# Optimization experiments

Hardware: AMD Instinct MI355X
Metric: run time of the kernel (lower is better)

Reference implementation:

```python
import jax, jax.numpy as jnp
import numpy as np

B, G, MAXITER = 8, 1024, 16
H = 1.0 / (G - 1)          # grid spacing h = (right-left)/(GridSize-1) on unit square
GD = 0.0                   # Dirichlet boundary value used by hard_encode padding

_K_CROSS = np.array([[0.0, 0.5, 0.0], [0.5, 0.0, 0.5], [0.0, 0.5, 0.0]], np.float32).reshape(1, 1, 3, 3)
_K3 = np.array([[0.0, 0.5, 0.0], [0.5, 2.0, 0.5], [0.0, 0.5, 0.0]], np.float32).reshape(1, 1, 3, 3)


def _conv3x3(x, k):
    # valid 3x3 conv, NCHW / OIHW (matches torch F.conv2d with no padding)
    return jax.lax.conv_general_dilated(x, k, (1, 1), 'VALID',
                                        dimension_numbers=('NCHW', 'OIHW', 'NCHW'))


def setup_inputs() -> dict:
    key = jax.random.key(0)
    k1, k2, k3 = jax.random.split(key, 3)
    pre = jax.random.normal(k1, (B, 1, G - 2, G - 2), dtype=jnp.float32)
    f = jax.random.normal(k2, (B, 1, G, G), dtype=jnp.float32)
    # positive coefficient field so the Jacobi divisor y3 stays bounded away from 0
    kappa = jax.random.uniform(k3, (B, 1, G, G), dtype=jnp.float32, minval=0.5, maxval=1.5)
    return {"pre": pre, "f": f, "kappa": kappa}


def reference(pre, f, kappa):
    kc = jnp.asarray(_K_CROSS, dtype=pre.dtype)
    k3 = jnp.asarray(_K3, dtype=pre.dtype)
    # loop-invariant terms: force = f_interior * h^2, w_interior, y3 = conv(w, k3)
    force = f[..., 1:-1, 1:-1] * (H * H)          # [B,1,G-2,G-2]
    w_in = kappa[..., 1:-1, 1:-1]                 # [B,1,G-2,G-2]
    y3 = _conv3x3(kappa, k3)                      # [B,1,G-2,G-2]

    def step(u, _):
        up = jnp.pad(u, ((0, 0), (0, 0), (1, 1), (1, 1)), constant_values=GD)  # hard_encode
        y1 = _conv3x3(up, kc) * w_in
        y2 = _conv3x3(kappa * up, kc)
        return (force + y1 + y2) / y3, None

    u, _ = jax.lax.scan(step, pre, None, length=MAXITER)
    return u
```

## Files before the change

### kernel.cpp

```cpp
#include <hip/hip_runtime.h>


namespace {
constexpr int    G    = 1024, Ni = 1022;
constexpr int    TOUT = 96, HALO = 16;
constexpr size_t IMG_K = (size_t)G * G;
constexpr size_t IMG_P = (size_t)Ni * Ni;
constexpr float  H2 = (float)(1.0 / (1023.0 * 1023.0));
}

__device__ __forceinline__ float frcp(float x) { return __builtin_amdgcn_rcpf(x); }

__device__ __forceinline__ float lane_shr1(float x) {
    return __builtin_bit_cast(float,
        __builtin_amdgcn_update_dpp(0, __builtin_bit_cast(int, x), 0x138, 0xF, 0xF, true));
}
__device__ __forceinline__ float lane_shl1(float x) {
    return __builtin_bit_cast(float,
        __builtin_amdgcn_update_dpp(0, __builtin_bit_cast(int, x), 0x130, 0xF, 0xF, true));
}

__global__ __launch_bounds__(1024, 4)
void jac_fused16(const float* __restrict__ pre, float* __restrict__ out,
                 const float* __restrict__ kap, const float* __restrict__ fin)
{
    __shared__ float2 ex[2][2][1024];

    const int tid = threadIdx.x;
    const int w = tid >> 6, l = tid & 63;
    const int bx = blockIdx.x, by = blockIdx.y, b = blockIdx.z;
    const int X0 = bx * TOUT - HALO, Y0 = by * TOUT - HALO;
    const int c0 = X0 + 2 * l;
    const int gy0 = Y0 + 8 * w;

    const float* kB = kap + (size_t)b * IMG_K;
    const float* fB = fin + (size_t)b * IMG_K;
    const bool fast = (bx >= 1) && (bx <= 9) && (by >= 1) && (by <= 9);

    float2 wN[8], wS[8], wW[8], wE[8], Fc[8];
    if (fast) {
        const float* kp = kB + (size_t)gy0 * G + c0;
        const float* fp = fB + (size_t)(gy0 + 1) * G + c0;
        float2 q0 = *(const float2*)kp;
        float2 q1 = *(const float2*)(kp + G);
        float  e0 = lane_shl1(q0.x);
        float  e1 = lane_shl1(q1.x);
        #pragma unroll
        for (int r = 0; r < 8; ++r) {
            const float2 q2 = *(const float2*)(kp + (size_t)(r + 2) * G);
            const float  e2 = lane_shl1(q2.x);
            const float2 fr = *(const float2*)(fp + (size_t)r * G);
            const float f0 = fr.y, f1 = lane_shl1(fr.x);
            const float ke1 = lane_shl1(q1.y);
            const float inv0 = frcp(2.0f * q1.y + 0.5f * (q0.y + q2.y + q1.x + e1));
            const float inv1 = frcp(2.0f * e1   + 0.5f * (e0 + e2 + q1.y + ke1));
            wN[r] = make_float2(0.5f * (q1.y + q0.y) * inv0, 0.5f * (e1 + e0) * inv1);
            wS[r] = make_float2(0.5f * (q1.y + q2.y) * inv0, 0.5f * (e1 + e2) * inv1);
            wW[r] = make_float2(0.5f * (q1.y + q1.x) * inv0, 0.5f * (e1 + q1.y) * inv1);
            wE[r] = make_float2(0.5f * (q1.y + e1)   * inv0, 0.5f * (e1 + ke1) * inv1);
            Fc[r] = make_float2(f0 * H2 * inv0, f1 * H2 * inv1);
            q0 = q1; q1 = q2; e0 = e1; e1 = e2;
        }
    } else {
        auto gk = [&](int ry, int cx) -> float {
            return ((unsigned)ry < (unsigned)G && (unsigned)cx < (unsigned)G)
                 ? kB[(size_t)ry * G + cx] : 0.0f;
        };
        float qx0 = gk(gy0,     c0), qy0 = gk(gy0,     c0 + 1);
        float qx1 = gk(gy0 + 1, c0), qy1 = gk(gy0 + 1, c0 + 1);
        float e0 = lane_shl1(qx0), e1 = lane_shl1(qx1);
        #pragma unroll
        for (int r = 0; r < 8; ++r) {
            const float qx2 = gk(gy0 + r + 2, c0), qy2 = gk(gy0 + r + 2, c0 + 1);
            const float e2 = lane_shl1(qx2);
            const int ry = gy0 + 1 + r;
            const bool rv = (unsigned)ry < (unsigned)G;
            const float fa = (rv && (unsigned)c0       < (unsigned)G) ? fB[(size_t)ry * G + c0]     : 0.0f;
            const float fb = (rv && (unsigned)(c0 + 1) < (unsigned)G) ? fB[(size_t)ry * G + c0 + 1] : 0.0f;
            const float f0 = fb, f1 = lane_shl1(fa);
            const float ke1 = lane_shl1(qy1);
            const float inv0 = frcp(2.0f * qy1 + 0.5f * (qy0 + qy2 + qx1 + e1));
            const float inv1 = frcp(2.0f * e1  + 0.5f * (e0 + e2 + qy1 + ke1));
            const int gy = gy0 + r;
            const bool dr = (unsigned)gy < (unsigned)Ni;
            const bool d0 = dr && (unsigned)c0       < (unsigned)Ni;
            const bool d1 = dr && (unsigned)(c0 + 1) < (unsigned)Ni;
            wN[r] = make_float2(d0 ? 0.5f * (qy1 + qy0) * inv0 : 0.0f,
                                d1 ? 0.5f * (e1 + e0)   * inv1 : 0.0f);
            wS[r] = make_float2(d0 ? 0.5f * (qy1 + qy2) * inv0 : 0.0f,
                                d1 ? 0.5f * (e1 + e2)   * inv1 : 0.0f);
            wW[r] = make_float2(d0 ? 0.5f * (qy1 + qx1) * inv0 : 0.0f,
                                d1 ? 0.5f * (e1 + qy1)  * inv1 : 0.0f);
            wE[r] = make_float2(d0 ? 0.5f * (qy1 + e1)  * inv0 : 0.0f,
                                d1 ? 0.5f * (e1 + ke1)  * inv1 : 0.0f);
            Fc[r] = make_float2(d0 ? f0 * H2 * inv0 : 0.0f,
                                d1 ? f1 * H2 * inv1 : 0.0f);
            qx0 = qx1; qy0 = qy1; qx1 = qx2; qy1 = qy2; e0 = e1; e1 = e2;
        }
    }

    float2 u[8];
    if (fast) {
        const float* uS = pre + (size_t)b * IMG_P + (size_t)gy0 * Ni + c0;
        #pragma unroll
        for (int r = 0; r < 8; ++r) u[r] = *(const float2*)(uS + (size_t)r * Ni);
    } else {
        const float* uS = pre + (size_t)b * IMG_P;
        #pragma unroll
        for (int r = 0; r < 8; ++r) {
            const int gy = gy0 + r;
            const bool rv = (unsigned)gy < (unsigned)Ni;
            const float a = (rv && (unsigned)c0       < (unsigned)Ni) ? uS[(size_t)gy * Ni + c0]     : 0.0f;
            const float q = (rv && (unsigned)(c0 + 1) < (unsigned)Ni) ? uS[(size_t)gy * Ni + c0 + 1] : 0.0f;
            u[r] = make_float2(a, q);
        }
    }

    const int iN = (w > 0)  ? tid - 64 : tid;
    const int iS = (w < 15) ? tid + 64 : tid;
    #pragma unroll
    for (int t = 0; t < 16; ++t) {
        float2* top = ex[t & 1][0];
        float2* bot = ex[t & 1][1];
        top[tid] = u[0];
        bot[tid] = u[7];
        __syncthreads();
        const float2 hN = bot[iN];
        const float2 hS = top[iS];
        float2 pn = hN;
        #pragma unroll
        for (int r = 0; r < 8; ++r) {
            const float2 s = (r < 7) ? u[r + 1] : hS;
            const float o0 = u[r].x, o1 = u[r].y;
            const float uW = lane_shr1(o1);
            const float uE = lane_shl1(o0);
            const float v0 = fmaf(wN[r].x, pn.x,
                             fmaf(wS[r].x, s.x,
                             fmaf(wW[r].x, uW,
                             fmaf(wE[r].x, o1, Fc[r].x))));
            const float v1 = fmaf(wN[r].y, pn.y,
                             fmaf(wS[r].y, s.y,
                             fmaf(wW[r].y, o0,
                             fmaf(wE[r].y, uE, Fc[r].y))));
            pn = make_float2(o0, o1);
            u[r] = make_float2(v0, v1);
        }
    }

    if (w >= 2 && w < 14 && l >= 8 && l < 56) {
        float* oB = out + (size_t)b * IMG_P;
        if (fast) {
            #pragma unroll
            for (int r = 0; r < 8; ++r)
                *(float2*)(oB + (size_t)(gy0 + r) * Ni + c0) = u[r];
        } else {
            #pragma unroll
            for (int r = 0; r < 8; ++r) {
                const int gy = gy0 + r;
                if ((unsigned)gy < (unsigned)Ni) {
                    if ((unsigned)c0       < (unsigned)Ni) oB[(size_t)gy * Ni + c0]     = u[r].x;
                    if ((unsigned)(c0 + 1) < (unsigned)Ni) oB[(size_t)gy * Ni + c0 + 1] = u[r].y;
                }
            }
        }
    }
}

extern "C" void kernel_launch(void* const* d_in, const int* in_sizes, int n_in,
                              void* d_out, int out_size, void* d_ws, size_t ws_size,
                              hipStream_t stream)
{
    const float* pre = (const float*)d_in[0];
    const float* f   = (const float*)d_in[1];
    const float* kap = (const float*)d_in[2];
    float* out = (float*)d_out;
    (void)d_ws; (void)ws_size;

    dim3 blk(1024, 1, 1);
    dim3 grd((Ni + TOUT - 1) / TOUT, (Ni + TOUT - 1) / TOUT, 8);

    jac_fused16<<<grd, blk, 0, stream>>>(pre, out, kap, f);
}
```

Baseline: 197.5 us.

## Eliminate east stencil weight via unit-sum identity and relax launch bounds

The four Jacobi neighbour weights sum to one, so the east weight is dropped. Each update is rewritten as the east neighbour plus weighted differences to the other neighbours, which frees the per-row wE registers. Boundary tiles lose the zero-weight trick for the east term, so a per-element mask array and a separate masked instantiation of the time loop are added. The launch bounds change from a min-blocks hint to an explicit waves-per-EU of 4, changing the register budget the compiler targets. The cost is extra subtractions per point, slightly different rounding from the rcp-based weights, and the mask multiplies on boundary tiles.

```diff
diff --git a/kernel.cpp b/kernel.cpp
--- a/kernel.cpp
+++ b/kernel.cpp
@@ -20,7 +20,8 @@
         __builtin_amdgcn_update_dpp(0, __builtin_bit_cast(int, x), 0x130, 0xF, 0xF, true));
 }
 
-__global__ __launch_bounds__(1024, 4)
+__global__ __launch_bounds__(1024)
+__attribute__((amdgpu_waves_per_eu(4, 4)))
 void jac_fused16(const float* __restrict__ pre, float* __restrict__ out,
                  const float* __restrict__ kap, const float* __restrict__ fin)
 {
@@ -37,7 +38,8 @@
     const float* fB = fin + (size_t)b * IMG_K;
     const bool fast = (bx >= 1) && (bx <= 9) && (by >= 1) && (by <= 9);
 
-    float2 wN[8], wS[8], wW[8], wE[8], Fc[8];
+    float2 wN[8], wS[8], wW[8], Fc[8];
+    float2 mk[8];
     if (fast) {
         const float* kp = kB + (size_t)gy0 * G + c0;
         const float* fp = fB + (size_t)(gy0 + 1) * G + c0;
@@ -57,7 +59,6 @@
             wN[r] = make_float2(0.5f * (q1.y + q0.y) * inv0, 0.5f * (e1 + e0) * inv1);
             wS[r] = make_float2(0.5f * (q1.y + q2.y) * inv0, 0.5f * (e1 + e2) * inv1);
             wW[r] = make_float2(0.5f * (q1.y + q1.x) * inv0, 0.5f * (e1 + q1.y) * inv1);
-            wE[r] = make_float2(0.5f * (q1.y + e1)   * inv0, 0.5f * (e1 + ke1) * inv1);
             Fc[r] = make_float2(f0 * H2 * inv0, f1 * H2 * inv1);
             q0 = q1; q1 = q2; e0 = e1; e1 = e2;
         }
@@ -66,6 +67,8 @@
             return ((unsigned)ry < (unsigned)G && (unsigned)cx < (unsigned)G)
                  ? kB[(size_t)ry * G + cx] : 0.0f;
         };
+        const float cm0 = ((unsigned)c0       < (unsigned)Ni) ? 1.0f : 0.0f;
+        const float cm1 = ((unsigned)(c0 + 1) < (unsigned)Ni) ? 1.0f : 0.0f;
         float qx0 = gk(gy0,     c0), qy0 = gk(gy0,     c0 + 1);
         float qx1 = gk(gy0 + 1, c0), qy1 = gk(gy0 + 1, c0 + 1);
         float e0 = lane_shl1(qx0), e1 = lane_shl1(qx1);
@@ -91,10 +94,10 @@
                                 d1 ? 0.5f * (e1 + e2)   * inv1 : 0.0f);
             wW[r] = make_float2(d0 ? 0.5f * (qy1 + qx1) * inv0 : 0.0f,
                                 d1 ? 0.5f * (e1 + qy1)  * inv1 : 0.0f);
-            wE[r] = make_float2(d0 ? 0.5f * (qy1 + e1)  * inv0 : 0.0f,
-                                d1 ? 0.5f * (e1 + ke1)  * inv1 : 0.0f);
             Fc[r] = make_float2(d0 ? f0 * H2 * inv0 : 0.0f,
                                 d1 ? f1 * H2 * inv1 : 0.0f);
+            const float rmr = dr ? 1.0f : 0.0f;
+            mk[r] = make_float2(rmr * cm0, rmr * cm1);
             qx0 = qx1; qy0 = qy1; qx1 = qx2; qy1 = qy2; e0 = e1; e1 = e2;
         }
     }
@@ -118,34 +121,64 @@
 
     const int iN = (w > 0)  ? tid - 64 : tid;
     const int iS = (w < 15) ? tid + 64 : tid;
-    #pragma unroll
-    for (int t = 0; t < 16; ++t) {
-        float2* top = ex[t & 1][0];
-        float2* bot = ex[t & 1][1];
-        top[tid] = u[0];
-        bot[tid] = u[7];
-        __syncthreads();
-        const float2 hN = bot[iN];
-        const float2 hS = top[iS];
-        float2 pn = hN;
-        #pragma unroll
-        for (int r = 0; r < 8; ++r) {
-            const float2 s = (r < 7) ? u[r + 1] : hS;
-            const float o0 = u[r].x, o1 = u[r].y;
-            const float uW = lane_shr1(o1);
-            const float uE = lane_shl1(o0);
-            const float v0 = fmaf(wN[r].x, pn.x,
-                             fmaf(wS[r].x, s.x,
-                             fmaf(wW[r].x, uW,
-                             fmaf(wE[r].x, o1, Fc[r].x))));
-            const float v1 = fmaf(wN[r].y, pn.y,
-                             fmaf(wS[r].y, s.y,
-                             fmaf(wW[r].y, o0,
-                             fmaf(wE[r].y, uE, Fc[r].y))));
-            pn = make_float2(o0, o1);
-            u[r] = make_float2(v0, v1);
-        }
-    }
+
+    auto run = [&](bool masked) {
+        #pragma unroll
+        for (int t = 0; t < 16; ++t) {
+            float2* top = ex[t & 1][0];
+            float2* bot = ex[t & 1][1];
+            top[tid] = u[0];
+            bot[tid] = u[7];
+            __syncthreads();
+            const float2 hN = bot[iN];
+            const float2 hS = top[iS];
+            const float2 o1s = u[1], o6s = u[6];
+            float2 pn = u[0];
+            #pragma unroll
+            for (int r = 1; r < 7; ++r) {
+                const float2 s = u[r + 1];
+                const float o0 = u[r].x, o1 = u[r].y;
+                const float uWh = lane_shr1(o1);
+                const float uEh = lane_shl1(o0);
+                float v0 = fmaf(wW[r].x, uWh - o1,
+                           fmaf(wS[r].x, s.x - o1,
+                           fmaf(wN[r].x, pn.x - o1, Fc[r].x + o1)));
+                float v1 = fmaf(wW[r].y, o0 - uEh,
+                           fmaf(wS[r].y, s.y - uEh,
+                           fmaf(wN[r].y, pn.y - uEh, Fc[r].y + uEh)));
+                if (masked) { v0 *= mk[r].x; v1 *= mk[r].y; }
+                pn = make_float2(o0, o1);
+                u[r] = make_float2(v0, v1);
+            }
+            {
+                const float o0 = u[0].x, o1 = u[0].y;
+                const float uWh = lane_shr1(o1);
+                const float uEh = lane_shl1(o0);
+                float v0 = fmaf(wW[0].x, uWh - o1,
+                           fmaf(wS[0].x, o1s.x - o1,
+                           fmaf(wN[0].x, hN.x - o1, Fc[0].x + o1)));
+                float v1 = fmaf(wW[0].y, o0 - uEh,
+                           fmaf(wS[0].y, o1s.y - uEh,
+                           fmaf(wN[0].y, hN.y - uEh, Fc[0].y + uEh)));
+                if (masked) { v0 *= mk[0].x; v1 *= mk[0].y; }
+                u[0] = make_float2(v0, v1);
+            }
+            {
+                const float o0 = u[7].x, o1 = u[7].y;
+                const float uWh = lane_shr1(o1);
+                const float uEh = lane_shl1(o0);
+                float v0 = fmaf(wW[7].x, uWh - o1,
+                           fmaf(wS[7].x, hS.x - o1,
+                           fmaf(wN[7].x, o6s.x - o1, Fc[7].x + o1)));
+                float v1 = fmaf(wW[7].y, o0 - uEh,
+                           fmaf(wS[7].y, hS.y - uEh,
+                           fmaf(wN[7].y, o6s.y - uEh, Fc[7].y + uEh)));
+                if (masked) { v0 *= mk[7].x; v1 *= mk[7].y; }
+                u[7] = make_float2(v0, v1);
+            }
+        }
+    };
+    if (fast) run(false); else run(true);
 
     if (w >= 2 && w < 14 && l >= 8 && l < 56) {
         float* oB = out + (size_t)b * IMG_P;
```

Result: slower. 305.2 us (+54.6%).
